# Kernel optimization log

Hardware: AMD Instinct MI355X
Metric: run time of the kernel (lower is better)

Reference implementation:

```python
import jax, jax.numpy as jnp
import numpy as np

EPS = 1e-06


def setup_inputs() -> dict:
    key = jax.random.key(0)
    k1, k2, k3 = jax.random.split(key, 3)
    B, L, S, C = 128, 512, 512, 64
    q = jax.random.normal(k1, (B, L, C), dtype=jnp.float32)
    k = jax.random.normal(k2, (B, S, C), dtype=jnp.float32)
    labels = jax.random.randint(k3, (B, L, S), 0, 2, dtype=jnp.int64)
    return {"q": q, "k": k, "labels": labels}


def reference(q, k, labels):
    # sim: [B, L, S], mapped to (0, 1) via (1 + cos-like sim) / 2
    sim = (1.0 + jnp.einsum('blc,bsc->bls', q, k)) * 0.5

    # column-wise stats (over L) -> [B, S]; torch.std uses ddof=1 (unbiased)
    col = (jnp.max(sim, axis=1) - jnp.mean(sim, axis=1)) / jnp.std(sim, axis=1, ddof=1)
    sharp1 = jax.nn.softmax(col, axis=-1)  # [B, S]

    # row-wise stats (over S) -> [B, L]
    row = (jnp.max(sim, axis=2) - jnp.mean(sim, axis=2)) / jnp.std(sim, axis=2, ddof=1)
    sharp2 = jax.nn.softmax(row, axis=-1)  # [B, L]

    simc = jnp.clip(sim, EPS, 1.0 - EPS)
    nll = -jnp.log(simc)                    # [B, L, S]
    nll_neg = -jnp.log(1.0 - simc)          # [B, L, S]

    pos = (labels == 1).astype(sim.dtype)
    neg = (labels == 0).astype(sim.dtype)

    # masked sums per sample, weighted by sharpness (broadcast over rows/cols)
    loss1 = jnp.sum(nll * sharp1[:, None, :] * pos, axis=(1, 2))  # [B]
    loss2 = jnp.sum(nll * sharp2[:, :, None] * pos, axis=(1, 2))  # [B]
    loss3 = jnp.sum(nll_neg * neg, axis=(1, 2)) / jnp.sum(neg, axis=(1, 2))  # [B]

    losses = (loss1 + loss2) * 0.5 + loss3
    return (sharp1, jnp.mean(losses))
```

## Files before the change

kernel.cpp:

```cpp
#include <hip/hip_runtime.h>

#define EPSF 1e-6f

typedef _Float16 half8 __attribute__((ext_vector_type(8)));
typedef float f32x4 __attribute__((ext_vector_type(4)));

constexpr int B = 128, L = 512, S = 512, C = 64;
constexpr int TILE_R = 64;
constexpr int TILES  = L / TILE_R;
constexpr int CHUNK  = 64;
constexpr int NCHUNK = S / CHUNK;
constexpr int HALVES = 2;
constexpr int CPB    = NCHUNK / HALVES;

constexpr size_t WS_COLMAX = 0;
constexpr size_t WS_COLSUM = WS_COLMAX + (size_t)B * TILES * S;
constexpr size_t WS_COLSSQ = WS_COLSUM + (size_t)B * TILES * S;
constexpr size_t WS_COLP1  = WS_COLSSQ + (size_t)B * TILES * S;
constexpr size_t WS_ROWMAX = WS_COLP1  + (size_t)B * TILES * S;
constexpr size_t WS_ROWSUM = WS_ROWMAX + (size_t)B * L * HALVES;
constexpr size_t WS_ROWSSQ = WS_ROWSUM + (size_t)B * L * HALVES;
constexpr size_t WS_ROWP2  = WS_ROWSSQ + (size_t)B * L * HALVES;
constexpr size_t WS_NEGS   = WS_ROWP2  + (size_t)B * L * HALVES;
constexpr size_t WS_NEGC   = WS_NEGS   + (size_t)B * TILES * HALVES;
constexpr size_t WS_QF     = WS_NEGC   + (size_t)B * TILES * HALVES;
constexpr size_t WS_KF     = WS_QF     + (size_t)B * TILES * 4096;

__device__ inline void loadTile(const float* __restrict__ g, float4 v[4], int t)
{
    const float* src = g + (t >> 2) * 64 + (t & 3) * 16;
    v[0] = *(const float4*)(src);
    v[1] = *(const float4*)(src + 4);
    v[2] = *(const float4*)(src + 8);
    v[3] = *(const float4*)(src + 12);
}

__device__ inline void fragStore(const float4 v4[4], half8* dhi, half8* dlo, int t)
{
    const int row = t >> 2, c0 = (t & 3) * 16;
    const float v[16] = {v4[0].x, v4[0].y, v4[0].z, v4[0].w, v4[1].x, v4[1].y, v4[1].z, v4[1].w,
                         v4[2].x, v4[2].y, v4[2].z, v4[2].w, v4[3].x, v4[3].y, v4[3].z, v4[3].w};
#pragma unroll
    for (int o = 0; o < 2; ++o) {
        const int cb     = c0 + o * 8;
        const int idx    = (row >> 4) * 2 + (cb >> 5);
        const int lane_s = (((cb >> 3) & 3) << 4) + (row & 15);
        half8 h, l;
#pragma unroll
        for (int j = 0; j < 8; ++j) {
            float f = v[o * 8 + j];
            _Float16 hi = (_Float16)f;
            h[j] = hi;
            l[j] = (_Float16)(f - (float)hi);
        }
        dhi[idx * 64 + lane_s] = h;
        dlo[idx * 64 + lane_s] = l;
    }
}

__global__ __launch_bounds__(256)
void convert_kernel(const float* __restrict__ q, const float* __restrict__ kmat,
                    float* __restrict__ ws)
{
    const int bidx = blockIdx.x;
    const int b    = bidx >> 4;
    const int t16  = bidx & 15;
    const int tid  = threadIdx.x;
    const bool isq = (t16 < TILES);
    const int tile = isq ? t16 : t16 - TILES;

    const float* src = isq ? (q    + ((size_t)b * L + (size_t)tile * TILE_R) * C)
                           : (kmat + ((size_t)b * S + (size_t)tile * CHUNK)  * C);
    half8* base = (half8*)(ws + (isq ? WS_QF : WS_KF)) + (size_t)(b * TILES + tile) * 1024;

    float4 v[4];
    loadTile(src, v, tid);
    fragStore(v, base, base + 512, tid);
}

__device__ inline void gl16(const void* g, void* l)
{
    __builtin_amdgcn_global_load_lds((const __attribute__((address_space(1))) void*)g,
                                     (__attribute__((address_space(3))) void*)l, 16, 0, 0);
}

__global__ __launch_bounds__(256) __attribute__((amdgpu_waves_per_eu(3, 8)))
void pass1_kernel(const int* __restrict__ labels, float* __restrict__ ws)
{
    __shared__ half8 kbuf[2][1024];
    __shared__ float4 colred4[4][CPB][CHUNK];
    __shared__ float nred[4][2];

    const int bidx = blockIdx.x;
    const int b    = bidx / (TILES * HALVES);
    const int rem  = bidx % (TILES * HALVES);
    const int tile = rem >> 1;
    const int half = rem & 1;
    const int chbase = half * CPB;
    const int tid  = threadIdx.x;
    const int lane = tid & 63;
    const int wave = tid >> 6;
    const int l15  = lane & 15;
    const int quad = lane >> 4;
    const int rowbase = tile * TILE_R;

    float* colmax_p = ws + WS_COLMAX;
    float* colsum_p = ws + WS_COLSUM;
    float* colssq_p = ws + WS_COLSSQ;
    float* colp1_p  = ws + WS_COLP1;
    float* rowmax_p = ws + WS_ROWMAX;
    float* rowsum_p = ws + WS_ROWSUM;
    float* rowssq_p = ws + WS_ROWSSQ;
    float* rowp2_p  = ws + WS_ROWP2;
    float* negs_p   = ws + WS_NEGS;
    float* negc_p   = ws + WS_NEGC;

    const int* lb = labels + ((size_t)b * L + rowbase) * S;

    const half8* qf  = (const half8*)(ws + WS_QF) + (size_t)(b * TILES + tile) * 1024;
    const half8* kf0 = (const half8*)(ws + WS_KF) + (size_t)b * NCHUNK * 1024;

    auto stage = [&](int ch, int bi) {
#pragma unroll
        for (int i = 0; i < 4; ++i)
            gl16(kf0 + (size_t)ch * 1024 + i * 256 + tid,
                 &kbuf[bi][i * 256 + (tid & 192)]);
    };

    stage(chbase, 0);

    half8 ah0 = qf[(wave * 2 + 0) * 64 + lane];
    half8 ah1 = qf[(wave * 2 + 1) * 64 + lane];
    half8 al0 = qf[512 + (wave * 2 + 0) * 64 + lane];
    half8 al1 = qf[512 + (wave * 2 + 1) * 64 + lane];

    int labn[16];
#pragma unroll
    for (int ct = 0; ct < 4; ++ct)
#pragma unroll
        for (int r = 0; r < 4; ++r)
            labn[ct * 4 + r] = __builtin_nontemporal_load(
                &lb[(size_t)(wave * 16 + quad * 4 + r) * S + chbase * CHUNK + ct * 16 + l15]);

    float rmax[4], rsum[4], rssq[4], rp2[4];
#pragma unroll
    for (int i = 0; i < 4; ++i) { rmax[i] = -3.4e38f; rsum[i] = 0.f; rssq[i] = 0.f; rp2[i] = 0.f; }
    float negsum = 0.f;
    int   possum = 0;

    __syncthreads();

    for (int c4 = 0; c4 < CPB; ++c4) {
        const int ch = chbase + c4;
        if (c4 + 1 < CPB) stage(ch + 1, (c4 + 1) & 1);
        const half8* kb = kbuf[c4 & 1];

        f32x4 acc[4];
#pragma unroll
        for (int ct = 0; ct < 4; ++ct) {
            half8 bh0 = kb[(ct * 2 + 0) * 64 + lane];
            half8 bh1 = kb[(ct * 2 + 1) * 64 + lane];
            half8 bl0 = kb[512 + (ct * 2 + 0) * 64 + lane];
            half8 bl1 = kb[512 + (ct * 2 + 1) * 64 + lane];
            f32x4 a = {0.f, 0.f, 0.f, 0.f};
            a = __builtin_amdgcn_mfma_f32_16x16x32_f16(ah0, bh0, a, 0, 0, 0);
            a = __builtin_amdgcn_mfma_f32_16x16x32_f16(ah0, bl0, a, 0, 0, 0);
            a = __builtin_amdgcn_mfma_f32_16x16x32_f16(al0, bh0, a, 0, 0, 0);
            a = __builtin_amdgcn_mfma_f32_16x16x32_f16(ah1, bh1, a, 0, 0, 0);
            a = __builtin_amdgcn_mfma_f32_16x16x32_f16(ah1, bl1, a, 0, 0, 0);
            a = __builtin_amdgcn_mfma_f32_16x16x32_f16(al1, bh1, a, 0, 0, 0);
            acc[ct] = a;
        }

#pragma unroll
        for (int ct = 0; ct < 4; ++ct) {
            float cmax = -3.4e38f, csum = 0.f, cssq = 0.f, cp1 = 0.f;
#pragma unroll
            for (int r = 0; r < 4; ++r) {
                int lab = labn[ct * 4 + r];
                float sim = fmaf(0.5f, acc[ct][r], 0.5f);
                rmax[r] = fmaxf(rmax[r], sim);
                rsum[r] += sim;
                rssq[r] = fmaf(sim, sim, rssq[r]);
                cmax = fmaxf(cmax, sim);
                csum += sim;
                cssq = fmaf(sim, sim, cssq);
                float sc  = fminf(fmaxf(sim, EPSF), 1.f - EPSF);
                bool  isp = (lab == 1);
                float pos = isp ? 1.f : 0.f;
                float t   = isp ? sc : (1.f - sc);
                float nl  = -__logf(t);
                float pn  = pos * nl;
                rp2[r] += pn;
                cp1 += pn;
                negsum += nl - pn;
                possum += lab;
            }
#pragma unroll
            for (int m = 16; m <= 32; m <<= 1) {
                cmax = fmaxf(cmax, __shfl_xor(cmax, m, 64));
                csum += __shfl_xor(csum, m, 64);
                cssq += __shfl_xor(cssq, m, 64);
                cp1  += __shfl_xor(cp1,  m, 64);
            }
            if (lane < 16)
                colred4[wave][c4][ct * 16 + l15] = make_float4(cmax, csum, cssq, cp1);
        }

        if (c4 + 1 < CPB) {
#pragma unroll
            for (int ct = 0; ct < 4; ++ct)
#pragma unroll
                for (int r = 0; r < 4; ++r)
                    labn[ct * 4 + r] = __builtin_nontemporal_load(
                        &lb[(size_t)(wave * 16 + quad * 4 + r) * S + (ch + 1) * CHUNK + ct * 16 + l15]);
        }

        __syncthreads();
    }

    {
        const int cc  = tid >> 6;
        const int col = tid & 63;
        float4 v = colred4[0][cc][col];
        float m0 = v.x, s1 = v.y, s2 = v.z, pp = v.w;
#pragma unroll
        for (int w = 1; w < 4; ++w) {
            float4 u = colred4[w][cc][col];
            m0 = fmaxf(m0, u.x); s1 += u.y; s2 += u.z; pp += u.w;
        }
        size_t idx = ((size_t)b * TILES + tile) * S + (chbase + cc) * CHUNK + col;
        colmax_p[idx] = m0; colsum_p[idx] = s1; colssq_p[idx] = s2; colp1_p[idx] = pp;
    }

#pragma unroll
    for (int r = 0; r < 4; ++r) {
#pragma unroll
        for (int m = 1; m <= 8; m <<= 1) {
            rmax[r] = fmaxf(rmax[r], __shfl_xor(rmax[r], m, 64));
            rsum[r] += __shfl_xor(rsum[r], m, 64);
            rssq[r] += __shfl_xor(rssq[r], m, 64);
            rp2[r]  += __shfl_xor(rp2[r],  m, 64);
        }
    }
    if (l15 == 0) {
#pragma unroll
        for (int r = 0; r < 4; ++r) {
            size_t idx = ((size_t)b * L + rowbase + wave * 16 + quad * 4 + r) * HALVES + half;
            rowmax_p[idx] = rmax[r]; rowsum_p[idx] = rsum[r];
            rowssq_p[idx] = rssq[r]; rowp2_p[idx]  = rp2[r];
        }
    }

    float negcnt = (float)(16 * CPB - possum);
#pragma unroll
    for (int m = 1; m <= 32; m <<= 1) {
        negsum += __shfl_xor(negsum, m, 64);
        negcnt += __shfl_xor(negcnt, m, 64);
    }
    if (lane == 0) { nred[wave][0] = negsum; nred[wave][1] = negcnt; }
    __syncthreads();
    if (tid == 0) {
        float ns = 0.f, nc = 0.f;
        for (int w = 0; w < 4; ++w) { ns += nred[w][0]; nc += nred[w][1]; }
        negs_p[bidx] = ns; negc_p[bidx] = nc;
    }
}

template <bool MAX>
__device__ inline float bred(float v, float* red)
{
#pragma unroll
    for (int m = 1; m <= 32; m <<= 1) {
        float o = __shfl_xor(v, m, 64);
        v = MAX ? fmaxf(v, o) : (v + o);
    }
    const int wave = threadIdx.x >> 6;
    const int lane = threadIdx.x & 63;
    if (lane == 0) red[wave] = v;
    __syncthreads();
    if (threadIdx.x == 0) {
        float r = red[0];
        for (int w = 1; w < 8; ++w) r = MAX ? fmaxf(r, red[w]) : (r + red[w]);
        red[8] = r;
    }
    __syncthreads();
    float out = red[8];
    __syncthreads();
    return out;
}

__global__ __launch_bounds__(512)
void pass2_kernel(const float* __restrict__ ws, float* __restrict__ out)
{
    __shared__ float red[9];
    const int b = blockIdx.x;
    const int s = threadIdx.x;

    if (blockIdx.y == 0) {
        const float* colmax_p = ws + WS_COLMAX;
        const float* colsum_p = ws + WS_COLSUM;
        const float* colssq_p = ws + WS_COLSSQ;
        const float* colp1_p  = ws + WS_COLP1;

        float m = -3.4e38f, sm = 0.f, sq = 0.f, p1 = 0.f;
#pragma unroll
        for (int t = 0; t < TILES; ++t) {
            size_t idx = ((size_t)b * TILES + t) * S + s;
            m = fmaxf(m, colmax_p[idx]);
            sm += colsum_p[idx];
            sq += colssq_p[idx];
            p1 += colp1_p[idx];
        }
        float mean  = sm * (1.f / L);
        float var   = (sq - sm * sm * (1.f / L)) * (1.f / (L - 1));
        float score = (m - mean) / sqrtf(var);

        float gmax = bred<true>(score, red);
        float e    = __expf(score - gmax);
        float esum = bred<false>(e, red);
        float sharp1 = e / esum;
        out[(size_t)b * S + s] = sharp1;
        float loss1 = bred<false>(sharp1 * p1, red);
        if (s == 0) atomicAdd(out + (size_t)B * S, loss1 * (0.5f / B));
    } else {
        const float* rowmax_p = ws + WS_ROWMAX;
        const float* rowsum_p = ws + WS_ROWSUM;
        const float* rowssq_p = ws + WS_ROWSSQ;
        const float* rowp2_p  = ws + WS_ROWP2;
        const float* negs_p   = ws + WS_NEGS;
        const float* negc_p   = ws + WS_NEGC;

        size_t ridx = ((size_t)b * L + s) * HALVES;
        float m2 = rowmax_p[ridx], sm2 = rowsum_p[ridx];
        float sq2 = rowssq_p[ridx], p2 = rowp2_p[ridx];
#pragma unroll
        for (int h = 1; h < HALVES; ++h) {
            m2 = fmaxf(m2, rowmax_p[ridx + h]);
            sm2 += rowsum_p[ridx + h];
            sq2 += rowssq_p[ridx + h];
            p2  += rowp2_p[ridx + h];
        }
        float mean2  = sm2 * (1.f / S);
        float var2   = (sq2 - sm2 * sm2 * (1.f / S)) * (1.f / (S - 1));
        float score2 = (m2 - mean2) / sqrtf(var2);

        float gmax2 = bred<true>(score2, red);
        float e2    = __expf(score2 - gmax2);
        float esum2 = bred<false>(e2, red);
        float loss2 = bred<false>((e2 / esum2) * p2, red);

        if (s == 0) {
            float ns = 0.f, nc = 0.f;
            for (int t = 0; t < TILES * HALVES; ++t) {
                ns += negs_p[b * TILES * HALVES + t];
                nc += negc_p[b * TILES * HALVES + t];
            }
            atomicAdd(out + (size_t)B * S, (0.5f * loss2 + ns / nc) * (1.f / B));
        }
    }
}

extern "C" void kernel_launch(void* const* d_in, const int* in_sizes, int n_in,
                              void* d_out, int out_size, void* d_ws, size_t ws_size,
                              hipStream_t stream)
{
    const float* q      = (const float*)d_in[0];
    const float* k      = (const float*)d_in[1];
    const int*   labels = (const int*)d_in[2];
    float* out = (float*)d_out;
    float* ws  = (float*)d_ws;

    hipMemsetAsync((char*)d_out + (size_t)B * S * sizeof(float), 0, sizeof(float), stream);

    convert_kernel<<<dim3(B * (TILES + NCHUNK)), dim3(256), 0, stream>>>(q, k, ws);
    pass1_kernel<<<dim3(B * TILES * HALVES), dim3(256), 0, stream>>>(labels, ws);
    pass2_kernel<<<dim3(B, 2), dim3(512), 0, stream>>>(ws, out);
}
```

Before: 251.9 us.

## Pre-pack labels into bitmasks in convert kernel before pass1

Adds a pre-pass inside the convert kernel that reads the int labels and packs them into 64-bit ballot bitmasks per row chunk in workspace. Pass1 then reads one 64-bit word per row per chunk instead of 16 int loads per lane, and extracts each label with a shift. The full label array is still read once, but the label traffic inside the MFMA-heavy pass1 loop shrinks sharply. The cost is an extra write/read of the small packed array and more blocks in the convert launch, and the original prefetch of labels one chunk ahead is removed.

Result: slower. 271.4 us (+7.7%).

```diff
diff --git a/kernel.cpp b/kernel.cpp
--- a/kernel.cpp
+++ b/kernel.cpp
@@ -25,6 +25,11 @@
 constexpr size_t WS_NEGC   = WS_NEGS   + (size_t)B * TILES * HALVES;
 constexpr size_t WS_QF     = WS_NEGC   + (size_t)B * TILES * HALVES;
 constexpr size_t WS_KF     = WS_QF     + (size_t)B * TILES * 4096;
+constexpr size_t WS_LP     = WS_KF     + (size_t)B * NCHUNK * 4096;
+
+constexpr int PACK_ROWS   = 4;
+constexpr int CONV_BLOCKS = B * (TILES + NCHUNK);
+constexpr int PACK_BLOCKS = B * L / PACK_ROWS;
 
 __device__ inline void loadTile(const float* __restrict__ g, float4 v[4], int t)
 {
@@ -60,22 +65,42 @@
 
 __global__ __launch_bounds__(256)
 void convert_kernel(const float* __restrict__ q, const float* __restrict__ kmat,
-                    float* __restrict__ ws)
+                    const int* __restrict__ labels, float* __restrict__ ws)
 {
     const int bidx = blockIdx.x;
-    const int b    = bidx >> 4;
-    const int t16  = bidx & 15;
     const int tid  = threadIdx.x;
-    const bool isq = (t16 < TILES);
-    const int tile = isq ? t16 : t16 - TILES;
-
-    const float* src = isq ? (q    + ((size_t)b * L + (size_t)tile * TILE_R) * C)
-                           : (kmat + ((size_t)b * S + (size_t)tile * CHUNK)  * C);
-    half8* base = (half8*)(ws + (isq ? WS_QF : WS_KF)) + (size_t)(b * TILES + tile) * 1024;
-
-    float4 v[4];
-    loadTile(src, v, tid);
-    fragStore(v, base, base + 512, tid);
+
+    if (bidx < CONV_BLOCKS) {
+        const int b    = bidx >> 4;
+        const int t16  = bidx & 15;
+        const bool isq = (t16 < TILES);
+        const int tile = isq ? t16 : t16 - TILES;
+
+        const float* src = isq ? (q    + ((size_t)b * L + (size_t)tile * TILE_R) * C)
+                               : (kmat + ((size_t)b * S + (size_t)tile * CHUNK)  * C);
+        half8* base = (half8*)(ws + (isq ? WS_QF : WS_KF)) + (size_t)(b * TILES + tile) * 1024;
+
+        float4 v[4];
+        loadTile(src, v, tid);
+        fragStore(v, base, base + 512, tid);
+    } else {
+        const int pb   = bidx - CONV_BLOCKS;
+        const int b    = pb / (L / PACK_ROWS);
+        const int rg   = pb % (L / PACK_ROWS);
+        const int wave = tid >> 6, lane = tid & 63;
+        const size_t row = (size_t)b * L + rg * PACK_ROWS + wave;
+        const int* src = labels + row * S;
+        unsigned long long* dst = (unsigned long long*)(ws + WS_LP) + row * 8;
+        int v[8];
+#pragma unroll
+        for (int w = 0; w < 8; ++w)
+            v[w] = __builtin_nontemporal_load(&src[w * 64 + lane]);
+#pragma unroll
+        for (int w = 0; w < 8; ++w) {
+            unsigned long long m = __ballot(v[w] == 1);
+            if (lane == 0) dst[w] = m;
+        }
+    }
 }
 
 __device__ inline void gl16(const void* g, void* l)
@@ -85,7 +110,7 @@
 }
 
 __global__ __launch_bounds__(256) __attribute__((amdgpu_waves_per_eu(3, 8)))
-void pass1_kernel(const int* __restrict__ labels, float* __restrict__ ws)
+void pass1_kernel(float* __restrict__ ws)
 {
     __shared__ half8 kbuf[2][1024];
     __shared__ float4 colred4[4][CPB][CHUNK];
@@ -115,10 +140,10 @@
     float* negs_p   = ws + WS_NEGS;
     float* negc_p   = ws + WS_NEGC;
 
-    const int* lb = labels + ((size_t)b * L + rowbase) * S;
-
     const half8* qf  = (const half8*)(ws + WS_QF) + (size_t)(b * TILES + tile) * 1024;
     const half8* kf0 = (const half8*)(ws + WS_KF) + (size_t)b * NCHUNK * 1024;
+    const unsigned long long* lp =
+        (const unsigned long long*)(ws + WS_LP) + ((size_t)b * L + rowbase) * 8;
 
     auto stage = [&](int ch, int bi) {
 #pragma unroll
@@ -134,14 +159,6 @@
     half8 al0 = qf[512 + (wave * 2 + 0) * 64 + lane];
     half8 al1 = qf[512 + (wave * 2 + 1) * 64 + lane];
 
-    int labn[16];
-#pragma unroll
-    for (int ct = 0; ct < 4; ++ct)
-#pragma unroll
-        for (int r = 0; r < 4; ++r)
-            labn[ct * 4 + r] = __builtin_nontemporal_load(
-                &lb[(size_t)(wave * 16 + quad * 4 + r) * S + chbase * CHUNK + ct * 16 + l15]);
-
     float rmax[4], rsum[4], rssq[4], rp2[4];
 #pragma unroll
     for (int i = 0; i < 4; ++i) { rmax[i] = -3.4e38f; rsum[i] = 0.f; rssq[i] = 0.f; rp2[i] = 0.f; }
@@ -154,6 +171,11 @@
         const int ch = chbase + c4;
         if (c4 + 1 < CPB) stage(ch + 1, (c4 + 1) & 1);
         const half8* kb = kbuf[c4 & 1];
+
+        unsigned long long lw[4];
+#pragma unroll
+        for (int r = 0; r < 4; ++r)
+            lw[r] = lp[(size_t)(wave * 16 + quad * 4 + r) * 8 + ch];
 
         f32x4 acc[4];
 #pragma unroll
@@ -177,7 +199,7 @@
             float cmax = -3.4e38f, csum = 0.f, cssq = 0.f, cp1 = 0.f;
 #pragma unroll
             for (int r = 0; r < 4; ++r) {
-                int lab = labn[ct * 4 + r];
+                int lab = (int)((lw[r] >> (ct * 16 + l15)) & 1ull);
                 float sim = fmaf(0.5f, acc[ct][r], 0.5f);
                 rmax[r] = fmaxf(rmax[r], sim);
                 rsum[r] += sim;
@@ -207,15 +229,6 @@
                 colred4[wave][c4][ct * 16 + l15] = make_float4(cmax, csum, cssq, cp1);
         }
 
-        if (c4 + 1 < CPB) {
-#pragma unroll
-            for (int ct = 0; ct < 4; ++ct)
-#pragma unroll
-                for (int r = 0; r < 4; ++r)
-                    labn[ct * 4 + r] = __builtin_nontemporal_load(
-                        &lb[(size_t)(wave * 16 + quad * 4 + r) * S + (ch + 1) * CHUNK + ct * 16 + l15]);
-        }
-
         __syncthreads();
     }
 
@@ -373,7 +386,7 @@
 
     hipMemsetAsync((char*)d_out + (size_t)B * S * sizeof(float), 0, sizeof(float), stream);
 
-    convert_kernel<<<dim3(B * (TILES + NCHUNK)), dim3(256), 0, stream>>>(q, k, ws);
-    pass1_kernel<<<dim3(B * TILES * HALVES), dim3(256), 0, stream>>>(labels, ws);
+    convert_kernel<<<dim3(CONV_BLOCKS + PACK_BLOCKS), dim3(256), 0, stream>>>(q, k, labels, ws);
+    pass1_kernel<<<dim3(B * TILES * HALVES), dim3(256), 0, stream>>>(ws);
     pass2_kernel<<<dim3(B, 2), dim3(512), 0, stream>>>(ws, out);
 }
```

## Preload labels as bitmasks, fuse MFMA with epilogue, pipeline column reduction

Applied to the files above, without the earlier changes.

Loads all label values for the block upfront and packs them into per-chunk bitmasks, so the later per-chunk label reloads go away and fewer registers are live. The MFMA and the stats epilogue now share one loop per column tile, and the chunk loop is fully unrolled. The cross-wave column reduction moves into a two-slot LDS ring that is drained one chunk late, overlapping its global stores with the next chunk's compute and shrinking shared memory. It also raises the minimum waves-per-EU hint to 4 and folds the output memset into convert_kernel, removing one API call, at the cost of register pressure and a larger up-front label load.

New measurement: 358.4 us. 42.3% more time.

```diff
diff --git a/kernel.cpp b/kernel.cpp
--- a/kernel.cpp
+++ b/kernel.cpp
@@ -26,6 +26,8 @@
 constexpr size_t WS_QF     = WS_NEGC   + (size_t)B * TILES * HALVES;
 constexpr size_t WS_KF     = WS_QF     + (size_t)B * TILES * 4096;
 
+constexpr int CONV_BLOCKS = B * (TILES + NCHUNK);
+
 __device__ inline void loadTile(const float* __restrict__ g, float4 v[4], int t)
 {
     const float* src = g + (t >> 2) * 64 + (t & 3) * 16;
@@ -60,12 +62,14 @@
 
 __global__ __launch_bounds__(256)
 void convert_kernel(const float* __restrict__ q, const float* __restrict__ kmat,
-                    float* __restrict__ ws)
+                    float* __restrict__ ws, float* __restrict__ out)
 {
     const int bidx = blockIdx.x;
+    const int tid  = threadIdx.x;
+    if (bidx == 0 && tid == 0) out[(size_t)B * S] = 0.f;
+
     const int b    = bidx >> 4;
     const int t16  = bidx & 15;
-    const int tid  = threadIdx.x;
     const bool isq = (t16 < TILES);
     const int tile = isq ? t16 : t16 - TILES;
 
@@ -84,12 +88,11 @@
                                      (__attribute__((address_space(3))) void*)l, 16, 0, 0);
 }
 
-__global__ __launch_bounds__(256) __attribute__((amdgpu_waves_per_eu(3, 8)))
+__global__ __launch_bounds__(256) __attribute__((amdgpu_waves_per_eu(4, 8)))
 void pass1_kernel(const int* __restrict__ labels, float* __restrict__ ws)
 {
     __shared__ half8 kbuf[2][1024];
-    __shared__ float4 colred4[4][CPB][CHUNK];
-    __shared__ float nred[4][2];
+    __shared__ float4 colring[2][4][CHUNK];
 
     const int bidx = blockIdx.x;
     const int b    = bidx / (TILES * HALVES);
@@ -134,28 +137,51 @@
     half8 al0 = qf[512 + (wave * 2 + 0) * 64 + lane];
     half8 al1 = qf[512 + (wave * 2 + 1) * 64 + lane];
 
-    int labn[16];
-#pragma unroll
-    for (int ct = 0; ct < 4; ++ct)
-#pragma unroll
-        for (int r = 0; r < 4; ++r)
-            labn[ct * 4 + r] = __builtin_nontemporal_load(
-                &lb[(size_t)(wave * 16 + quad * 4 + r) * S + chbase * CHUNK + ct * 16 + l15]);
+    unsigned labm[CPB];
+#pragma unroll
+    for (int cc = 0; cc < CPB; ++cc) {
+        unsigned m = 0;
+#pragma unroll
+        for (int ct = 0; ct < 4; ++ct)
+#pragma unroll
+            for (int r = 0; r < 4; ++r) {
+                int lab = __builtin_nontemporal_load(
+                    &lb[(size_t)(wave * 16 + quad * 4 + r) * S
+                        + (chbase + cc) * CHUNK + ct * 16 + l15]);
+                m |= (unsigned)(lab == 1) << (ct * 4 + r);
+            }
+        labm[cc] = m;
+    }
 
     float rmax[4], rsum[4], rssq[4], rp2[4];
 #pragma unroll
     for (int i = 0; i < 4; ++i) { rmax[i] = -3.4e38f; rsum[i] = 0.f; rssq[i] = 0.f; rp2[i] = 0.f; }
     float negsum = 0.f;
-    int   possum = 0;
-
-    __syncthreads();
-
+
+    __syncthreads();
+
+#pragma unroll
     for (int c4 = 0; c4 < CPB; ++c4) {
         const int ch = chbase + c4;
         if (c4 + 1 < CPB) stage(ch + 1, (c4 + 1) & 1);
+
+        if (c4 > 0 && lane < 16) {
+            const int col  = wave * 16 + l15;
+            const int slot = (c4 - 1) & 1;
+            float4 v = colring[slot][0][col];
+            float m0 = v.x, s1 = v.y, s2 = v.z, pp = v.w;
+#pragma unroll
+            for (int w = 1; w < 4; ++w) {
+                float4 u = colring[slot][w][col];
+                m0 = fmaxf(m0, u.x); s1 += u.y; s2 += u.z; pp += u.w;
+            }
+            size_t idx = ((size_t)b * TILES + tile) * S + (size_t)(ch - 1) * CHUNK + col;
+            colmax_p[idx] = m0; colsum_p[idx] = s1; colssq_p[idx] = s2; colp1_p[idx] = pp;
+        }
+
         const half8* kb = kbuf[c4 & 1];
-
-        f32x4 acc[4];
+        const unsigned lm = labm[c4];
+
 #pragma unroll
         for (int ct = 0; ct < 4; ++ct) {
             half8 bh0 = kb[(ct * 2 + 0) * 64 + lane];
@@ -169,16 +195,12 @@
             a = __builtin_amdgcn_mfma_f32_16x16x32_f16(ah1, bh1, a, 0, 0, 0);
             a = __builtin_amdgcn_mfma_f32_16x16x32_f16(ah1, bl1, a, 0, 0, 0);
             a = __builtin_amdgcn_mfma_f32_16x16x32_f16(al1, bh1, a, 0, 0, 0);
-            acc[ct] = a;
-        }
-
-#pragma unroll
-        for (int ct = 0; ct < 4; ++ct) {
+
             float cmax = -3.4e38f, csum = 0.f, cssq = 0.f, cp1 = 0.f;
 #pragma unroll
             for (int r = 0; r < 4; ++r) {
-                int lab = labn[ct * 4 + r];
-                float sim = fmaf(0.5f, acc[ct][r], 0.5f);
+                int lab = (int)((lm >> (ct * 4 + r)) & 1u);
+                float sim = fmaf(0.5f, a[r], 0.5f);
                 rmax[r] = fmaxf(rmax[r], sim);
                 rsum[r] += sim;
                 rssq[r] = fmaf(sim, sim, rssq[r]);
@@ -194,7 +216,6 @@
                 rp2[r] += pn;
                 cp1 += pn;
                 negsum += nl - pn;
-                possum += lab;
             }
 #pragma unroll
             for (int m = 16; m <= 32; m <<= 1) {
@@ -204,32 +225,23 @@
                 cp1  += __shfl_xor(cp1,  m, 64);
             }
             if (lane < 16)
-                colred4[wave][c4][ct * 16 + l15] = make_float4(cmax, csum, cssq, cp1);
-        }
-
-        if (c4 + 1 < CPB) {
-#pragma unroll
-            for (int ct = 0; ct < 4; ++ct)
-#pragma unroll
-                for (int r = 0; r < 4; ++r)
-                    labn[ct * 4 + r] = __builtin_nontemporal_load(
-                        &lb[(size_t)(wave * 16 + quad * 4 + r) * S + (ch + 1) * CHUNK + ct * 16 + l15]);
+                colring[c4 & 1][wave][ct * 16 + l15] = make_float4(cmax, csum, cssq, cp1);
         }
 
         __syncthreads();
     }
 
-    {
-        const int cc  = tid >> 6;
-        const int col = tid & 63;
-        float4 v = colred4[0][cc][col];
+    if (lane < 16) {
+        const int col  = wave * 16 + l15;
+        const int slot = (CPB - 1) & 1;
+        float4 v = colring[slot][0][col];
         float m0 = v.x, s1 = v.y, s2 = v.z, pp = v.w;
 #pragma unroll
         for (int w = 1; w < 4; ++w) {
-            float4 u = colred4[w][cc][col];
+            float4 u = colring[slot][w][col];
             m0 = fmaxf(m0, u.x); s1 += u.y; s2 += u.z; pp += u.w;
         }
-        size_t idx = ((size_t)b * TILES + tile) * S + (chbase + cc) * CHUNK + col;
+        size_t idx = ((size_t)b * TILES + tile) * S + (size_t)(chbase + CPB - 1) * CHUNK + col;
         colmax_p[idx] = m0; colsum_p[idx] = s1; colssq_p[idx] = s2; colp1_p[idx] = pp;
     }
 
@@ -252,17 +264,19 @@
         }
     }
 
+    int possum = __popc(labm[0]) + __popc(labm[1]) + __popc(labm[2]) + __popc(labm[3]);
     float negcnt = (float)(16 * CPB - possum);
 #pragma unroll
     for (int m = 1; m <= 32; m <<= 1) {
         negsum += __shfl_xor(negsum, m, 64);
         negcnt += __shfl_xor(negcnt, m, 64);
     }
-    if (lane == 0) { nred[wave][0] = negsum; nred[wave][1] = negcnt; }
+    float* nscr = (float*)colring;
+    if (lane == 0) { nscr[wave * 2] = negsum; nscr[wave * 2 + 1] = negcnt; }
     __syncthreads();
     if (tid == 0) {
         float ns = 0.f, nc = 0.f;
-        for (int w = 0; w < 4; ++w) { ns += nred[w][0]; nc += nred[w][1]; }
+        for (int w = 0; w < 4; ++w) { ns += nscr[w * 2]; nc += nscr[w * 2 + 1]; }
         negs_p[bidx] = ns; negc_p[bidx] = nc;
     }
 }
@@ -371,9 +385,7 @@
     float* out = (float*)d_out;
     float* ws  = (float*)d_ws;
 
-    hipMemsetAsync((char*)d_out + (size_t)B * S * sizeof(float), 0, sizeof(float), stream);
-
-    convert_kernel<<<dim3(B * (TILES + NCHUNK)), dim3(256), 0, stream>>>(q, k, ws);
+    convert_kernel<<<dim3(CONV_BLOCKS), dim3(256), 0, stream>>>(q, k, ws, out);
     pass1_kernel<<<dim3(B * TILES * HALVES), dim3(256), 0, stream>>>(labels, ws);
     pass2_kernel<<<dim3(B, 2), dim3(512), 0, stream>>>(ws, out);
 }
```
